# Kernel optimization log

Hardware: AMD Instinct MI355X
Metric: run time of the kernel (lower is better)

The kernel has to match this reference:

```python
import jax, jax.numpy as jnp
import numpy as np
from jax import lax

VOCAB, EMB, HID, LAYERS, BATCH, SEQ = 32000, 512, 512, 2, 32, 64


def setup_inputs() -> dict:
    key = jax.random.key(0)
    ks = jax.random.split(key, 10)
    s = 0.05
    return {
        "input_seq": jax.random.normal(ks[0], (BATCH, SEQ, EMB), jnp.float32),
        "h_encode": jax.random.normal(ks[1], (LAYERS, BATCH, HID), jnp.float32),
        "c_encode": jax.random.normal(ks[2], (LAYERS, BATCH, HID), jnp.float32),
        # stacked LSTM cell params (E == H so layer 0 stacks with the rest)
        "Wih": jax.random.normal(ks[3], (LAYERS, 4 * HID, EMB), jnp.float32) * s,
        "Whh": jax.random.normal(ks[4], (LAYERS, 4 * HID, HID), jnp.float32) * s,
        "bih": jax.random.normal(ks[5], (LAYERS, 4 * HID), jnp.float32) * s,
        "bhh": jax.random.normal(ks[6], (LAYERS, 4 * HID), jnp.float32) * s,
        # output projection fc: Linear(hidden_size, output_size)
        "fcW": jax.random.normal(ks[7], (VOCAB, HID), jnp.float32) * s,
        "fcb": jax.random.normal(ks[8], (VOCAB,), jnp.float32) * s,
        # tgt_embedding table [vocab, input_size]
        "emb": jax.random.normal(ks[9], (VOCAB, EMB), jnp.float32) * s,
    }


def _cell(x, h, c, wih, whh, bi, bh):
    # standard LSTM cell: gates = x Wih^T + h Whh^T + biases, order (i, f, g, o)
    g = x @ wih.T + bi + h @ whh.T + bh
    i, f, gg, o = jnp.split(g, 4, axis=-1)
    c_new = jax.nn.sigmoid(f) * c + jax.nn.sigmoid(i) * jnp.tanh(gg)
    h_new = jax.nn.sigmoid(o) * jnp.tanh(c_new)
    return h_new, c_new


def reference(input_seq, h_encode, c_encode, Wih, Whh, bih, bhh, fcW, fcb, emb):
    B, S, _ = input_seq.shape
    L = Whh.shape[0]

    def step(carry, _):
        x, h, c = carry  # x: [B,E], h/c: [L,B,H]
        hs, cs = [], []
        inp = x
        for l in range(L):  # small fixed layer count
            hh, cc = _cell(inp, h[l], c[l], Wih[l], Whh[l], bih[l], bhh[l])
            hs.append(hh)
            cs.append(cc)
            inp = hh
        out = inp @ fcW.T + fcb  # [B, VOCAB] logits
        nxt = emb[jnp.argmax(out, axis=1)]  # [B, E]
        return (nxt, jnp.stack(hs), jnp.stack(cs)), out

    init = (input_seq[:, 0, :], h_encode, c_encode)
    _, outs = lax.scan(step, init, None, length=S)  # outs: [S, B, V]
    return jnp.transpose(outs, (1, 0, 2))  # [B, S, V]
```

## Files before the change

kernel.cpp:

```cpp
#include <hip/hip_runtime.h>
#include <math.h>


#define BB   32
#define EMBD 512
#define HIDD 512
#define VV   32000
#define SS   64
#define GJ   2048
#define OST  (SS*VV)

__device__ __forceinline__ float sigf(float x){ return 1.0f/(1.0f + expf(-x)); }
__device__ __forceinline__ unsigned keyOf(float f){
  unsigned u = __float_as_uint(f);
  return (u & 0x80000000u) ? ~u : (u | 0x80000000u);
}

__global__ void ktran(const float* __restrict__ src, float* __restrict__ dst,
                      int R, int C, int dstLd)
{
  __shared__ float t[32][33];
  int c0 = blockIdx.x*32, r0 = blockIdx.y*32;
  int tx = threadIdx.x & 31, ty = threadIdx.x >> 5;
  #pragma unroll
  for (int i=0;i<4;i++) t[ty+i*8][tx] = src[(size_t)(r0+ty+i*8)*C + (c0+tx)];
  __syncthreads();
  #pragma unroll
  for (int i=0;i<4;i++) dst[(size_t)(c0+ty+i*8)*dstLd + (r0+tx)] = t[tx][ty+i*8];
}

__global__ void kbias(const float* __restrict__ bih, const float* __restrict__ bhh,
                      float* __restrict__ bias2){
  int i = blockIdx.x*256 + threadIdx.x;
  if (i < 2*GJ) bias2[i] = bih[i] + bhh[i];
}

__global__ void kinit(const float* __restrict__ iseq, const float* __restrict__ he,
                      const float* __restrict__ ce, float* __restrict__ x0T,
                      float* __restrict__ hT, float* __restrict__ cT)
{
  int tid = blockIdx.x*256 + threadIdx.x;
  if (tid < 16384){
    int k = tid>>5, b = tid&31;
    x0T[tid] = iseq[(size_t)b*(SS*EMBD) + k];
  } else if (tid < 49152){
    int t2 = tid - 16384;
    int l = t2>>14, r = t2&16383, u = r>>5, b = r&31;
    hT[t2] = he[(size_t)(l*BB + b)*HIDD + u];
  } else if (tid < 81920){
    int t2 = tid - 49152;
    int l = t2>>14, r = t2&16383, u = r>>5, b = r&31;
    cT[t2] = ce[(size_t)(l*BB + b)*HIDD + u];
  }
}

__global__ __launch_bounds__(256) void klstm(
    const float* __restrict__ W2T, const float* __restrict__ bias2,
    const float* __restrict__ xsrc, const unsigned long long* __restrict__ slots_prev,
    const float* __restrict__ emb,
    const float* __restrict__ hsrc, const float* __restrict__ csrc,
    float* __restrict__ hdst, float* __restrict__ cdst,
    float* __restrict__ part, unsigned* __restrict__ ctr, int use_emb)
{
  __shared__ float xg[128*32];
  __shared__ float red[4*32*65];
  __shared__ int isLast;
  int bx = blockIdx.x;
  int jt = bx & 31, ko = bx >> 5;
  int tid = threadIdx.x, lane = tid & 63, kc = tid >> 6;
  int j = jt*64 + lane;

  if (ko >= 4){
    const float* base = hsrc + (size_t)(ko-4)*128*BB;
    #pragma unroll
    for (int i=0;i<4;i++)
      *(float4*)&xg[(i*256+tid)*4] = *(const float4*)(base + (size_t)(i*256+tid)*4);
  } else if (!use_emb){
    const float* base = xsrc + (size_t)ko*128*BB;
    #pragma unroll
    for (int i=0;i<4;i++)
      *(float4*)&xg[(i*256+tid)*4] = *(const float4*)(base + (size_t)(i*256+tid)*4);
  } else {
    int gb = tid & 31, kt = tid >> 5;
    unsigned long long pk = slots_prev[gb];
    unsigned idx = 0xFFFFFFFFu - (unsigned)(pk & 0xFFFFFFFFull);
    const float* row = emb + (size_t)idx*EMBD + ko*128 + kt*16;
    #pragma unroll
    for (int q=0;q<4;q++){
      float4 r4 = *(const float4*)(row + q*4);
      xg[(kt*16+q*4+0)*32 + gb] = r4.x;
      xg[(kt*16+q*4+1)*32 + gb] = r4.y;
      xg[(kt*16+q*4+2)*32 + gb] = r4.z;
      xg[(kt*16+q*4+3)*32 + gb] = r4.w;
    }
  }
  __syncthreads();

  float acc[BB];
  #pragma unroll
  for (int b=0;b<BB;b++) acc[b] = 0.f;

  const float* wp = W2T + (size_t)(ko*128 + kc*32)*GJ + j;
  const float* xb = &xg[(kc*32)*32];
  for (int kk=0;kk<32;kk++){
    float w = wp[(size_t)kk*GJ];
    const float* xr = xb + kk*32;
    #pragma unroll
    for (int bq=0;bq<8;bq++){
      float4 xa = *(const float4*)(xr + bq*4);
      acc[bq*4+0] = fmaf(xa.x, w, acc[bq*4+0]);
      acc[bq*4+1] = fmaf(xa.y, w, acc[bq*4+1]);
      acc[bq*4+2] = fmaf(xa.z, w, acc[bq*4+2]);
      acc[bq*4+3] = fmaf(xa.w, w, acc[bq*4+3]);
    }
  }

  #pragma unroll
  for (int b=0;b<BB;b++) red[(kc*32+b)*65 + lane] = acc[b];
  __syncthreads();

  #pragma unroll
  for (int i=0;i<8;i++){
    int idx = i*256 + tid, jl = idx >> 5, b2 = idx & 31;
    float v = red[(0*32+b2)*65 + jl] + red[(1*32+b2)*65 + jl]
            + red[(2*32+b2)*65 + jl] + red[(3*32+b2)*65 + jl];
    part[((size_t)ko*GJ + jt*64 + jl)*BB + b2] = v;
  }
  __threadfence();
  __syncthreads();
  int ug = jt & 7;
  if (tid == 0) isLast = (atomicAdd(&ctr[ug], 1u) == 31u);
  __syncthreads();
  if (!isLast) return;

  if (tid == 0) ctr[ug] = 0;
  __threadfence();
  const int u0 = ug*64;
  for (int i=0;i<8;i++){
    int cid = i*256 + tid;
    int u = cid >> 5, b2 = cid & 31;
    int uu = u0 + u;
    float gi=0.f, gf=0.f, gg=0.f, go=0.f;
    #pragma unroll
    for (int k2=0;k2<8;k2++){
      const float* pp = part + (size_t)k2*GJ*BB;
      gi += pp[(size_t)(0*512+uu)*BB + b2];
      gf += pp[(size_t)(1*512+uu)*BB + b2];
      gg += pp[(size_t)(2*512+uu)*BB + b2];
      go += pp[(size_t)(3*512+uu)*BB + b2];
    }
    gi += bias2[uu]; gf += bias2[512+uu]; gg += bias2[1024+uu]; go += bias2[1536+uu];
    float co = csrc[uu*BB + b2];
    float cn = sigf(gf)*co + sigf(gi)*tanhf(gg);
    float hn = sigf(go)*tanhf(cn);
    cdst[uu*BB + b2] = cn;
    hdst[uu*BB + b2] = hn;
  }
}

__global__ __launch_bounds__(256) void kfc(
    const float* __restrict__ fcWT, const float* __restrict__ fcb,
    const float* __restrict__ h1T, float* __restrict__ out, int s,
    unsigned long long* __restrict__ slots_cur,
    unsigned long long* __restrict__ slots_next)
{
  __shared__ float smem[16384];
  float* part0 = smem;
  float* part1 = smem + 4224;
  float* fin   = smem + 8448;
  int bx = blockIdx.x;
  int tid = threadIdx.x, lane = tid & 63, kc = tid >> 6;
  int c0 = lane*2;
  int v0 = bx*128 + c0;

  #pragma unroll
  for (int i=0;i<16;i++)
    ((float4*)smem)[i*256 + tid] = ((const float4*)h1T)[i*256 + tid];
  __syncthreads();

  float acc0[BB], acc1[BB];
  #pragma unroll
  for (int b=0;b<BB;b++){ acc0[b] = 0.f; acc1[b] = 0.f; }

  const float2* wp = (const float2*)(fcWT + (size_t)(kc*128)*VV) + (v0 >> 1);
  const float*  hx = smem + (kc*128)*32;
  #pragma unroll 16
  for (int kk=0;kk<128;kk++){
    float2 w = wp[(size_t)kk*(VV/2)];
    const float* xr = hx + kk*32;
    #pragma unroll
    for (int bq=0;bq<8;bq++){
      float4 xa = *(const float4*)(xr + bq*4);
      acc0[bq*4+0] = fmaf(xa.x, w.x, acc0[bq*4+0]);
      acc1[bq*4+0] = fmaf(xa.x, w.y, acc1[bq*4+0]);
      acc0[bq*4+1] = fmaf(xa.y, w.x, acc0[bq*4+1]);
      acc1[bq*4+1] = fmaf(xa.y, w.y, acc1[bq*4+1]);
      acc0[bq*4+2] = fmaf(xa.z, w.x, acc0[bq*4+2]);
      acc1[bq*4+2] = fmaf(xa.z, w.y, acc1[bq*4+2]);
      acc0[bq*4+3] = fmaf(xa.w, w.x, acc0[bq*4+3]);
      acc1[bq*4+3] = fmaf(xa.w, w.y, acc1[bq*4+3]);
    }
  }
  __syncthreads();

  if (kc < 2){
    float* p = (kc == 0) ? part0 : part1;
    #pragma unroll
    for (int b=0;b<BB;b++){ p[(c0+0)*33 + b] = acc0[b]; p[(c0+1)*33 + b] = acc1[b]; }
  }
  __syncthreads();
  if (kc >= 2){
    float* p = (kc == 2) ? part0 : part1;
    #pragma unroll
    for (int b=0;b<BB;b++){ p[(c0+0)*33 + b] += acc0[b]; p[(c0+1)*33 + b] += acc1[b]; }
  }
  __syncthreads();

  #pragma unroll
  for (int i=0;i<16;i++){
    int cl = (tid & 63) + 64*(i & 1);
    int b  = (tid >> 6) + 4*(i >> 1);
    float val = part0[cl*33 + b] + part1[cl*33 + b] + fcb[bx*128 + cl];
    out[(size_t)b*OST + (size_t)s*VV + bx*128 + cl] = val;
    fin[b*129 + cl] = val;
  }
  __syncthreads();

  if (tid < 32){
    int b = tid;
    float best = fin[b*129]; int bv = 0;
    for (int c=1; c<128; c++){
      float f = fin[b*129 + c];
      if (f > best){ best = f; bv = c; }
    }
    unsigned long long pk = ((unsigned long long)keyOf(best) << 32)
                          | (unsigned long long)(0xFFFFFFFFu - (unsigned)(bx*128 + bv));
    unsigned long long cur = slots_cur[b];
    if (pk > cur) atomicMax(slots_cur + b, pk);
  }
  if (bx == 0 && tid >= 64 && tid < 96) slots_next[tid - 64] = 0ull;
}

extern "C" void kernel_launch(void* const* d_in, const int* in_sizes, int n_in,
                              void* d_out, int out_size, void* d_ws, size_t ws_size,
                              hipStream_t stream)
{
  const float* input_seq = (const float*)d_in[0];
  const float* h_enc     = (const float*)d_in[1];
  const float* c_enc     = (const float*)d_in[2];
  const float* Wih       = (const float*)d_in[3];
  const float* Whh       = (const float*)d_in[4];
  const float* bih       = (const float*)d_in[5];
  const float* bhh       = (const float*)d_in[6];
  const float* fcW       = (const float*)d_in[7];
  const float* fcb       = (const float*)d_in[8];
  const float* emb       = (const float*)d_in[9];
  float* out = (float*)d_out;

  char* ws = (char*)d_ws;
  size_t off = 0;
  auto alloc = [&](size_t bytes)->void*{
    void* p = ws + off; off += (bytes + 255) & ~(size_t)255; return p;
  };
  float* fcWT  = (float*)alloc((size_t)512*VV*4);
  float* W2T   = (float*)alloc((size_t)2*1024*GJ*4);
  float* bias2 = (float*)alloc((size_t)2*GJ*4);
  float* x0T   = (float*)alloc((size_t)512*BB*4);
  float* hT    = (float*)alloc((size_t)2*2*512*BB*4);
  float* cT    = (float*)alloc((size_t)2*2*512*BB*4);
  float* partL0= (float*)alloc((size_t)8*GJ*BB*4);
  float* partL1= (float*)alloc((size_t)8*GJ*BB*4);
  unsigned long long* slots = (unsigned long long*)alloc(2*BB*8);
  unsigned* ctr = (unsigned*)alloc(16*4);

  hipMemsetAsync(slots, 0, 2*BB*8, stream);
  hipMemsetAsync(ctr,   0, 16*4,   stream);

  dim3 tb(256);
  ktran<<<dim3(16,1000), tb, 0, stream>>>(fcW, fcWT, VV, 512, VV);
  ktran<<<dim3(16,64), tb, 0, stream>>>(Wih,            W2T,                         GJ, 512, GJ);
  ktran<<<dim3(16,64), tb, 0, stream>>>(Whh,            W2T + (size_t)512*GJ,        GJ, 512, GJ);
  ktran<<<dim3(16,64), tb, 0, stream>>>(Wih + (size_t)GJ*512, W2T + (size_t)1024*GJ, GJ, 512, GJ);
  ktran<<<dim3(16,64), tb, 0, stream>>>(Whh + (size_t)GJ*512, W2T + (size_t)1024*GJ + (size_t)512*GJ, GJ, 512, GJ);
  kbias<<<16, tb, 0, stream>>>(bih, bhh, bias2);
  kinit<<<320, tb, 0, stream>>>(input_seq, h_enc, c_enc, x0T, hT, cT);

  const size_t LSZ = 512*BB;
  for (int s=0; s<SS; s++){
    int p = s & 1, q = p ^ 1;
    float* h0s = hT + (size_t)(p*2+0)*LSZ;  float* h0d = hT + (size_t)(q*2+0)*LSZ;
    float* h1s = hT + (size_t)(p*2+1)*LSZ;  float* h1d = hT + (size_t)(q*2+1)*LSZ;
    float* c0s = cT + (size_t)(p*2+0)*LSZ;  float* c0d = cT + (size_t)(q*2+0)*LSZ;
    float* c1s = cT + (size_t)(p*2+1)*LSZ;  float* c1d = cT + (size_t)(q*2+1)*LSZ;

    klstm<<<256, tb, 0, stream>>>(W2T, bias2,
        (s==0) ? x0T : nullptr,
        (s>0) ? (slots + ((s-1)&1)*BB) : nullptr,
        emb, h0s, c0s, h0d, c0d, partL0, ctr, (s>0) ? 1 : 0);
    klstm<<<256, tb, 0, stream>>>(W2T + (size_t)1024*GJ, bias2 + GJ,
        h0d, nullptr, emb, h1s, c1s, h1d, c1d, partL1, ctr + 8, 0);
    kfc<<<250, tb, 0, stream>>>(fcWT, fcb, h1d, out, s,
        slots + (s&1)*BB, slots + ((s+1)&1)*BB);
  }
}
```

Measured before the change: 7.733 ms.

## Double-buffer FC weight tiles through LDS with register prefetch

The output-projection kernel no longer streams fcW^T with per-iteration float2 global loads. Each wave now prefetches 16-row weight tiles into registers with float4 loads two tiles ahead and stages them into a per-wave double buffer in shared memory. This is meant to hide global-memory latency on the bandwidth-heavy vocabulary projection and widen the loads. In exchange, shared memory per block doubles to 128KB, which likely allows only one block per CU and lowers occupancy.

```diff
diff --git a/kernel.cpp b/kernel.cpp
--- a/kernel.cpp
+++ b/kernel.cpp
@@ -164,42 +164,68 @@
     unsigned long long* __restrict__ slots_cur,
     unsigned long long* __restrict__ slots_next)
 {
-  __shared__ float smem[16384];
+  __shared__ float smem[32768];
+  float* hs    = smem;
+  float* wt    = smem + 16384;
   float* part0 = smem;
   float* part1 = smem + 4224;
   float* fin   = smem + 8448;
   int bx = blockIdx.x;
   int tid = threadIdx.x, lane = tid & 63, kc = tid >> 6;
   int c0 = lane*2;
-  int v0 = bx*128 + c0;
+  const int kb0 = kc*128;
 
   #pragma unroll
   for (int i=0;i<16;i++)
-    ((float4*)smem)[i*256 + tid] = ((const float4*)h1T)[i*256 + tid];
+    ((float4*)hs)[i*256 + tid] = ((const float4*)h1T)[i*256 + tid];
+
+  float4 rg[8];
+  auto LOADR = [&](int t){
+    const float4* gp = (const float4*)(fcWT + (size_t)(kb0 + t*16)*VV) + (size_t)bx*32;
+    #pragma unroll
+    for (int q=0;q<8;q++){
+      int fi = q*64 + lane;
+      rg[q] = gp[(size_t)(fi>>5)*(VV/4) + (fi&31)];
+    }
+  };
+  auto WRITE = [&](int buf){
+    float* wb = wt + kc*4096 + buf*2048;
+    #pragma unroll
+    for (int q=0;q<8;q++){
+      int fi = q*64 + lane;
+      *(float4*)&wb[fi*4] = rg[q];
+    }
+  };
+
+  LOADR(0); WRITE(0); LOADR(1);
   __syncthreads();
 
   float acc0[BB], acc1[BB];
   #pragma unroll
   for (int b=0;b<BB;b++){ acc0[b] = 0.f; acc1[b] = 0.f; }
 
-  const float2* wp = (const float2*)(fcWT + (size_t)(kc*128)*VV) + (v0 >> 1);
-  const float*  hx = smem + (kc*128)*32;
-  #pragma unroll 16
-  for (int kk=0;kk<128;kk++){
-    float2 w = wp[(size_t)kk*(VV/2)];
-    const float* xr = hx + kk*32;
-    #pragma unroll
-    for (int bq=0;bq<8;bq++){
-      float4 xa = *(const float4*)(xr + bq*4);
-      acc0[bq*4+0] = fmaf(xa.x, w.x, acc0[bq*4+0]);
-      acc1[bq*4+0] = fmaf(xa.x, w.y, acc1[bq*4+0]);
-      acc0[bq*4+1] = fmaf(xa.y, w.x, acc0[bq*4+1]);
-      acc1[bq*4+1] = fmaf(xa.y, w.y, acc1[bq*4+1]);
-      acc0[bq*4+2] = fmaf(xa.z, w.x, acc0[bq*4+2]);
-      acc1[bq*4+2] = fmaf(xa.z, w.y, acc1[bq*4+2]);
-      acc0[bq*4+3] = fmaf(xa.w, w.x, acc0[bq*4+3]);
-      acc1[bq*4+3] = fmaf(xa.w, w.y, acc1[bq*4+3]);
-    }
+  for (int t=0; t<8; ++t){
+    const float* wb = wt + kc*4096 + (t&1)*2048;
+    const float* hx = hs + (kb0 + t*16)*32;
+    #pragma unroll
+    for (int kk=0;kk<16;kk++){
+      float2 w = *(const float2*)&wb[kk*128 + c0];
+      const float* xr = hx + kk*32;
+      #pragma unroll
+      for (int bq=0;bq<8;bq++){
+        float4 xa = *(const float4*)(xr + bq*4);
+        acc0[bq*4+0] = fmaf(xa.x, w.x, acc0[bq*4+0]);
+        acc1[bq*4+0] = fmaf(xa.x, w.y, acc1[bq*4+0]);
+        acc0[bq*4+1] = fmaf(xa.y, w.x, acc0[bq*4+1]);
+        acc1[bq*4+1] = fmaf(xa.y, w.y, acc1[bq*4+1]);
+        acc0[bq*4+2] = fmaf(xa.z, w.x, acc0[bq*4+2]);
+        acc1[bq*4+2] = fmaf(xa.z, w.y, acc1[bq*4+2]);
+        acc0[bq*4+3] = fmaf(xa.w, w.x, acc0[bq*4+3]);
+        acc1[bq*4+3] = fmaf(xa.w, w.y, acc1[bq*4+3]);
+      }
+    }
+    if (t+1 < 8) WRITE((t+1)&1);
+    if (t+2 < 8) LOADR(t+2);
   }
   __syncthreads();
 
```

Result: slower. 13.36 ms (+72.7%).
